# Kernel optimization log

Measured on AMD Instinct MI355X. Metric: run time of the kernel, lower is better.

Reference implementation:

```python
import jax, jax.numpy as jnp
import numpy as np

N_NODES = 50000
N_EDGES = 800000
NODE_F = 128
EDGE_F = 64
OUT_F = 128


def setup_inputs() -> dict:
    key = jax.random.key(0)
    k1, k2, k3, k4, k5 = jax.random.split(key, 5)
    x = jax.random.normal(k1, (N_NODES, NODE_F), dtype=jnp.float32)
    edge_index = jax.random.randint(k2, (2, N_EDGES), 0, N_NODES, dtype=jnp.int64)
    edge_attr = jax.random.normal(k3, (N_EDGES, EDGE_F), dtype=jnp.float32)
    # Linear(node_features + edge_features, out_features) params (torch default init scale)
    fan_in = NODE_F + EDGE_F
    bound = 1.0 / np.sqrt(fan_in)
    W = jax.random.uniform(k4, (fan_in, OUT_F), minval=-bound, maxval=bound, dtype=jnp.float32)
    b = jax.random.uniform(k5, (OUT_F,), minval=-bound, maxval=bound, dtype=jnp.float32)
    return {"x": x, "edge_index": edge_index, "edge_attr": edge_attr, "W": W, "b": b}


def reference(x, edge_index, edge_attr, W, b):
    # PyG source_to_target flow: x_j = x[src], aggregate at dst
    src = edge_index[0]
    dst = edge_index[1]
    x_j = x[src]                                   # [E, node_f] gather
    feats = jnp.concatenate([edge_attr, x_j], axis=1)  # [E, edge_f + node_f]
    msg = jax.nn.relu(feats @ W + b)               # [E, out_f] Linear + ReLU
    out = jax.ops.segment_sum(msg, dst, num_segments=x.shape[0])  # scatter-add
    return out
```

## Files before the change

### kernel.cpp

```cpp
#include <hip/hip_runtime.h>
#include <hip/hip_bf16.h>

#define N_NODES 50000
#define N_EDGES 800000
#define NODE_F  128
#define EDGE_F  64
#define OUT_F   128

#define NCH ((N_NODES + 255) / 256)
#define EPW 128
#define NRANGES (N_EDGES / EPW)

typedef __attribute__((ext_vector_type(8))) short short8;
typedef __attribute__((ext_vector_type(4))) short short4v;
typedef __attribute__((ext_vector_type(4))) float floatx4;

__device__ __forceinline__ unsigned short f2bf(float f) {
    unsigned int u = __float_as_uint(f);
    u += 0x7fffu + ((u >> 16) & 1u);
    return (unsigned short)(u >> 16);
}

__device__ __forceinline__ void load_bfrags(const float* __restrict__ W, int col, int quad,
                                            short8 bfr[2][8]) {
    #pragma unroll
    for (int kc = 0; kc < 2; ++kc) {
        #pragma unroll
        for (int ns = 0; ns < 8; ++ns) {
            const int n = ns * 16 + col;
            const int krow = kc * 32 + quad * 8;
            short8 v;
            #pragma unroll
            for (int j = 0; j < 8; ++j)
                v[j] = (short)f2bf(W[(krow + j) * OUT_F + n]);
            bfr[kc][ns] = v;
        }
    }
}

#define TILE_N1 32
#define N_NTILES ((N_NODES + TILE_N1 - 1) / TILE_N1)
#define LDS_STRIDE1 136

__global__ __launch_bounds__(256, 4) void node_kernel(
    const float* __restrict__ x,
    const float* __restrict__ W,
    const float* __restrict__ bias,
    float*       __restrict__ Y)
{
    __shared__ __align__(16) unsigned short xs[TILE_N1][LDS_STRIDE1];

    const int tid  = threadIdx.x;
    const int wave = tid >> 6;
    const int lane = tid & 63;
    const int col  = lane & 15;
    const int quad = lane >> 4;
    const int wbase = wave * 32;

    const float* __restrict__ Wx = W + EDGE_F * OUT_F;

    short8 bfr[4][2];
    #pragma unroll
    for (int kc = 0; kc < 4; ++kc) {
        #pragma unroll
        for (int ns = 0; ns < 2; ++ns) {
            const int n = wbase + ns * 16 + col;
            const int krow = kc * 32 + quad * 8;
            short8 v;
            #pragma unroll
            for (int j = 0; j < 8; ++j)
                v[j] = (short)f2bf(Wx[(krow + j) * OUT_F + n]);
            bfr[kc][ns] = v;
        }
    }
    const float b0 = bias[wbase + col];
    const float b1 = bias[wbase + 16 + col];

    for (int tile = blockIdx.x; tile < N_NTILES; tile += gridDim.x) {
        const int n0 = tile * TILE_N1;
        {
            const int e   = tid >> 3;
            const int sub = tid & 7;
            const int node = n0 + e;
            const float* __restrict__ xr = x + (size_t)node * NODE_F;
            #pragma unroll
            for (int i = 0; i < 4; ++i) {
                const int fi = sub + 8 * i;
                floatx4 v = {0.f, 0.f, 0.f, 0.f};
                if (node < N_NODES) v = *(const floatx4*)(xr + fi * 4);
                short4v sv;
                sv[0] = (short)f2bf(v[0]);
                sv[1] = (short)f2bf(v[1]);
                sv[2] = (short)f2bf(v[2]);
                sv[3] = (short)f2bf(v[3]);
                *(short4v*)&xs[e][fi * 4] = sv;
            }
        }
        __syncthreads();

        floatx4 acc[2][2] = {};
        #pragma unroll
        for (int kc = 0; kc < 4; ++kc) {
            short8 a0 = *(const short8*)&xs[col     ][kc * 32 + quad * 8];
            short8 a1 = *(const short8*)&xs[16 + col][kc * 32 + quad * 8];
            acc[0][0] = __builtin_amdgcn_mfma_f32_16x16x32_bf16(a0, bfr[kc][0], acc[0][0], 0, 0, 0);
            acc[0][1] = __builtin_amdgcn_mfma_f32_16x16x32_bf16(a0, bfr[kc][1], acc[0][1], 0, 0, 0);
            acc[1][0] = __builtin_amdgcn_mfma_f32_16x16x32_bf16(a1, bfr[kc][0], acc[1][0], 0, 0, 0);
            acc[1][1] = __builtin_amdgcn_mfma_f32_16x16x32_bf16(a1, bfr[kc][1], acc[1][1], 0, 0, 0);
        }

        #pragma unroll
        for (int ms = 0; ms < 2; ++ms) {
            #pragma unroll
            for (int r = 0; r < 4; ++r) {
                const int m = ms * 16 + quad * 4 + r;
                const int node = n0 + m;
                if (node < N_NODES) {
                    float* yrow = Y + (size_t)node * OUT_F + wbase;
                    yrow[col]      = acc[ms][0][r] + b0;
                    yrow[16 + col] = acc[ms][1][r] + b1;
                }
            }
        }
        __syncthreads();
    }
}

__global__ void hist_kernel(const int* __restrict__ edge_index, int* __restrict__ hist) {
    const int* dstp = edge_index + N_EDGES;
    for (int i = blockIdx.x * blockDim.x + threadIdx.x; i < N_EDGES;
         i += gridDim.x * blockDim.x)
        atomicAdd(&hist[dstp[i]], 1);
}

__global__ void scan1_kernel(const int* __restrict__ hist, int* __restrict__ chunkSum) {
    __shared__ int s[256];
    const int c = blockIdx.x, t = threadIdx.x, idx = c * 256 + t;
    s[t] = (idx < N_NODES) ? hist[idx] : 0;
    __syncthreads();
    for (int off = 128; off > 0; off >>= 1) {
        if (t < off) s[t] += s[t + off];
        __syncthreads();
    }
    if (t == 0) chunkSum[c] = s[0];
}

__global__ void scan2_kernel(const int* __restrict__ chunkSum, int* __restrict__ chunkBase) {
    __shared__ int s[256];
    const int t = threadIdx.x;
    s[t] = (t < NCH) ? chunkSum[t] : 0;
    __syncthreads();
    for (int off = 1; off < 256; off <<= 1) {
        int u = (t >= off) ? s[t - off] : 0;
        __syncthreads();
        s[t] += u;
        __syncthreads();
    }
    if (t < NCH) chunkBase[t] = (t == 0) ? 0 : s[t - 1];
}

__global__ void scan3_kernel(const int* __restrict__ hist, const int* __restrict__ chunkBase,
                             int* __restrict__ row_off, int* __restrict__ cursor) {
    __shared__ int s[256];
    const int c = blockIdx.x, t = threadIdx.x, idx = c * 256 + t;
    const int v = (idx < N_NODES) ? hist[idx] : 0;
    s[t] = v;
    __syncthreads();
    for (int off = 1; off < 256; off <<= 1) {
        int u = (t >= off) ? s[t - off] : 0;
        __syncthreads();
        s[t] += u;
        __syncthreads();
    }
    const int excl = s[t] - v + chunkBase[c];
    if (idx < N_NODES) { row_off[idx] = excl; cursor[idx] = excl; }
    if (c == 0 && t == 0) row_off[N_NODES] = N_EDGES;
}

__global__ void scatter_kernel(const int* __restrict__ edge_index,
                               int* __restrict__ cursor, int4* __restrict__ sorted) {
    const int* srcp = edge_index;
    const int* dstp = edge_index + N_EDGES;
    for (int i = blockIdx.x * blockDim.x + threadIdx.x; i < N_EDGES;
         i += gridDim.x * blockDim.x) {
        const int d = dstp[i];
        const int p = atomicAdd(&cursor[d], 1);
        sorted[p] = make_int4(i, srcp[i], d, 0);
    }
}

__device__ __forceinline__ int lbound(const int* __restrict__ ro, int target) {
    int lo = 0, hi = N_NODES;
    while (lo < hi) {
        const int mid = (lo + hi) >> 1;
        if (ro[mid] < target) lo = mid + 1; else hi = mid;
    }
    return lo;
}

__global__ __launch_bounds__(256, 3) void edge_gemm(
    const float* __restrict__ edge_attr,
    const float* __restrict__ W,
    const float* __restrict__ Y,
    const int*   __restrict__ row_off,
    const int4*  __restrict__ sorted,
    float*       __restrict__ out)
{
    __shared__ float CT[4][16][132];
    __shared__ int   drow[4][16];

    const int tid  = threadIdx.x;
    const int wave = tid >> 6;
    const int lane = tid & 63;
    const int col  = lane & 15;
    const int quad = lane >> 4;

    short8 bfr[2][8];
    load_bfrags(W, col, quad, bfr);

    const int gwave = blockIdx.x * 4 + wave;
    const int nw    = gridDim.x * 4;

    for (int rg = gwave; rg < NRANGES; rg += nw) {
        const int lo = lbound(row_off, rg * EPW);
        const int hi = lbound(row_off, (rg + 1) * EPW);
        const int eb = row_off[lo];
        const int ee = row_off[hi];
        if (eb >= ee) continue;

        int   cur = -1;
        float s0 = 0.f, s1 = 0.f;

        for (int t0 = eb; t0 < ee; t0 += 16) {
            const int cnt = min(16, ee - t0);

            int pa = t0 + col;
            if (pa >= ee) pa = ee - 1;
            const int4 me = sorted[pa];
            const float* __restrict__ ar = edge_attr + (size_t)me.x * EDGE_F;
            short8 a[2];
            #pragma unroll
            for (int kc = 0; kc < 2; ++kc) {
                floatx4 v0 = *(const floatx4*)(ar + kc * 32 + quad * 8);
                floatx4 v1 = *(const floatx4*)(ar + kc * 32 + quad * 8 + 4);
                short8 av;
                av[0] = (short)f2bf(v0[0]); av[1] = (short)f2bf(v0[1]);
                av[2] = (short)f2bf(v0[2]); av[3] = (short)f2bf(v0[3]);
                av[4] = (short)f2bf(v1[0]); av[5] = (short)f2bf(v1[1]);
                av[6] = (short)f2bf(v1[2]); av[7] = (short)f2bf(v1[3]);
                a[kc] = av;
            }

            if (lane < 16) drow[wave][lane] = (t0 + lane < ee) ? me.z : -1;

            const float* yrow[4];
            #pragma unroll
            for (int r = 0; r < 4; ++r) {
                int p = t0 + quad * 4 + r;
                if (p >= ee) p = ee - 1;
                yrow[r] = Y + (size_t)sorted[p].y * OUT_F;
            }

            floatx4 acc[8];
            #pragma unroll
            for (int ns = 0; ns < 8; ++ns) {
                #pragma unroll
                for (int r = 0; r < 4; ++r)
                    acc[ns][r] = yrow[r][ns * 16 + col];
            }

            #pragma unroll
            for (int kc = 0; kc < 2; ++kc) {
                #pragma unroll
                for (int ns = 0; ns < 8; ++ns)
                    acc[ns] = __builtin_amdgcn_mfma_f32_16x16x32_bf16(a[kc], bfr[kc][ns], acc[ns], 0, 0, 0);
            }

            #pragma unroll
            for (int ns = 0; ns < 8; ++ns) {
                #pragma unroll
                for (int r = 0; r < 4; ++r)
                    CT[wave][quad * 4 + r][ns * 16 + col] = fmaxf(acc[ns][r], 0.f);
            }
            __builtin_amdgcn_wave_barrier();

            for (int m = 0; m < cnt; ++m) {
                const int d = drow[wave][m];
                if (d != cur) {
                    if (cur >= 0) {
                        out[(size_t)cur * OUT_F + lane]      = s0;
                        out[(size_t)cur * OUT_F + 64 + lane] = s1;
                    }
                    cur = d; s0 = 0.f; s1 = 0.f;
                }
                s0 += CT[wave][m][lane];
                s1 += CT[wave][m][64 + lane];
            }
            __builtin_amdgcn_wave_barrier();
        }
        if (cur >= 0) {
            out[(size_t)cur * OUT_F + lane]      = s0;
            out[(size_t)cur * OUT_F + 64 + lane] = s1;
        }
    }
}

__global__ __launch_bounds__(256, 3) void edge_kernel_atomic(
    const float* __restrict__ edge_attr,
    const int*   __restrict__ edge_index,
    const float* __restrict__ W,
    const float* __restrict__ Y,
    float*       __restrict__ out)
{
    const int lane = threadIdx.x & 63;
    const int col  = lane & 15;
    const int quad = lane >> 4;

    short8 bfr[2][8];
    load_bfrags(W, col, quad, bfr);

    const int* __restrict__ srcp = edge_index;
    const int* __restrict__ dstp = edge_index + N_EDGES;

    const int gwave  = blockIdx.x * 4 + (threadIdx.x >> 6);
    const int nwaves = gridDim.x * 4;

    for (int t = gwave; t < N_EDGES / 16; t += nwaves) {
        const int e0 = t * 16;
        const float* __restrict__ ar = edge_attr + (size_t)(e0 + col) * EDGE_F;
        short8 a[2];
        #pragma unroll
        for (int kc = 0; kc < 2; ++kc) {
            floatx4 v0 = *(const floatx4*)(ar + kc * 32 + quad * 8);
            floatx4 v1 = *(const floatx4*)(ar + kc * 32 + quad * 8 + 4);
            short8 av;
            av[0] = (short)f2bf(v0[0]); av[1] = (short)f2bf(v0[1]);
            av[2] = (short)f2bf(v0[2]); av[3] = (short)f2bf(v0[3]);
            av[4] = (short)f2bf(v1[0]); av[5] = (short)f2bf(v1[1]);
            av[6] = (short)f2bf(v1[2]); av[7] = (short)f2bf(v1[3]);
            a[kc] = av;
        }
        int sr[4], dr[4];
        #pragma unroll
        for (int r = 0; r < 4; ++r) {
            sr[r] = srcp[e0 + quad * 4 + r];
            dr[r] = dstp[e0 + quad * 4 + r];
        }
        floatx4 acc[8];
        #pragma unroll
        for (int ns = 0; ns < 8; ++ns)
            #pragma unroll
            for (int r = 0; r < 4; ++r)
                acc[ns][r] = Y[(size_t)sr[r] * OUT_F + ns * 16 + col];
        #pragma unroll
        for (int kc = 0; kc < 2; ++kc)
            #pragma unroll
            for (int ns = 0; ns < 8; ++ns)
                acc[ns] = __builtin_amdgcn_mfma_f32_16x16x32_bf16(a[kc], bfr[kc][ns], acc[ns], 0, 0, 0);
        #pragma unroll
        for (int ns = 0; ns < 8; ++ns)
            #pragma unroll
            for (int r = 0; r < 4; ++r) {
                const float v = acc[ns][r];
                if (v > 0.0f)
                    atomicAdd(out + (size_t)dr[r] * OUT_F + ns * 16 + col, v);
            }
    }
}

extern "C" void kernel_launch(void* const* d_in, const int* in_sizes, int n_in,
                              void* d_out, int out_size, void* d_ws, size_t ws_size,
                              hipStream_t stream) {
    const float* x          = (const float*)d_in[0];
    const int*   edge_index = (const int*)  d_in[1];
    const float* edge_attr  = (const float*)d_in[2];
    const float* W          = (const float*)d_in[3];
    const float* bias       = (const float*)d_in[4];
    float*       out        = (float*)d_out;

    float* Y        = (float*)d_ws;
    int4*  sorted   = (int4*)(Y + (size_t)N_NODES * OUT_F);
    int*   hist     = (int*)(sorted + N_EDGES);
    int*   chunkSum = hist + N_NODES;
    int*   chunkBase= chunkSum + 256;
    int*   row_off  = chunkBase + 256;
    int*   cursor   = row_off + N_NODES + 1;
    const size_t needed = (size_t)((char*)(cursor + N_NODES) - (char*)d_ws);

    hipMemsetAsync(out, 0, (size_t)out_size * sizeof(float), stream);
    node_kernel<<<dim3(512), dim3(256), 0, stream>>>(x, W, bias, Y);

    if (ws_size < needed) {
        edge_kernel_atomic<<<dim3(1024), dim3(256), 0, stream>>>(edge_attr, edge_index, W, Y, out);
        return;
    }

    hipMemsetAsync(hist, 0, (size_t)N_NODES * sizeof(int), stream);
    hist_kernel   <<<dim3(2048), dim3(256), 0, stream>>>(edge_index, hist);
    scan1_kernel  <<<dim3(NCH),  dim3(256), 0, stream>>>(hist, chunkSum);
    scan2_kernel  <<<dim3(1),    dim3(256), 0, stream>>>(chunkSum, chunkBase);
    scan3_kernel  <<<dim3(NCH),  dim3(256), 0, stream>>>(hist, chunkBase, row_off, cursor);
    scatter_kernel<<<dim3(2048), dim3(256), 0, stream>>>(edge_index, cursor, sorted);
    edge_gemm     <<<dim3(1563), dim3(256), 0, stream>>>(edge_attr, W, Y, row_off, sorted, out);
}
```

Measured before the change: 516.2 us.

## Split edge GEMM columns across wave pairs, precompute range bounds, prefetch next tile

Each destination-sorted edge range is now handled by two waves, each computing 64 of the 128 output columns. This halves per-wave B fragments, accumulators and LDS, which allows a higher occupancy bound. The per-wave binary searches for range bounds move into a separate range_kernel. Inside the loop, dst ids are read via readlane instead of LDS, src indices are shuffled from the already loaded sorted entry, and the next tile's sorted entry and edge_attr are loaded early. The cost is duplicated edge_attr/sorted loads across the two waves and one extra small kernel launch.

```diff
diff --git a/kernel.cpp b/kernel.cpp
--- a/kernel.cpp
+++ b/kernel.cpp
@@ -19,23 +19,6 @@
     unsigned int u = __float_as_uint(f);
     u += 0x7fffu + ((u >> 16) & 1u);
     return (unsigned short)(u >> 16);
-}
-
-__device__ __forceinline__ void load_bfrags(const float* __restrict__ W, int col, int quad,
-                                            short8 bfr[2][8]) {
-    #pragma unroll
-    for (int kc = 0; kc < 2; ++kc) {
-        #pragma unroll
-        for (int ns = 0; ns < 8; ++ns) {
-            const int n = ns * 16 + col;
-            const int krow = kc * 32 + quad * 8;
-            short8 v;
-            #pragma unroll
-            for (int j = 0; j < 8; ++j)
-                v[j] = (short)f2bf(W[(krow + j) * OUT_F + n]);
-            bfr[kc][ns] = v;
-        }
-    }
 }
 
 #define TILE_N1 32
@@ -177,6 +160,20 @@
     if (c == 0 && t == 0) row_off[N_NODES] = N_EDGES;
 }
 
+__device__ __forceinline__ int lbound(const int* __restrict__ ro, int target) {
+    int lo = 0, hi = N_NODES;
+    while (lo < hi) {
+        const int mid = (lo + hi) >> 1;
+        if (ro[mid] < target) lo = mid + 1; else hi = mid;
+    }
+    return lo;
+}
+
+__global__ void range_kernel(const int* __restrict__ row_off, int* __restrict__ range_lo) {
+    const int rg = blockIdx.x * blockDim.x + threadIdx.x;
+    if (rg <= NRANGES) range_lo[rg] = lbound(row_off, rg * EPW);
+}
+
 __global__ void scatter_kernel(const int* __restrict__ edge_index,
                                int* __restrict__ cursor, int4* __restrict__ sorted) {
     const int* srcp = edge_index;
@@ -189,56 +186,54 @@
     }
 }
 
-__device__ __forceinline__ int lbound(const int* __restrict__ ro, int target) {
-    int lo = 0, hi = N_NODES;
-    while (lo < hi) {
-        const int mid = (lo + hi) >> 1;
-        if (ro[mid] < target) lo = mid + 1; else hi = mid;
-    }
-    return lo;
-}
-
-__global__ __launch_bounds__(256, 3) void edge_gemm(
+__global__ __launch_bounds__(256, 4) void edge_gemm(
     const float* __restrict__ edge_attr,
     const float* __restrict__ W,
     const float* __restrict__ Y,
     const int*   __restrict__ row_off,
+    const int*   __restrict__ range_lo,
     const int4*  __restrict__ sorted,
     float*       __restrict__ out)
 {
-    __shared__ float CT[4][16][132];
-    __shared__ int   drow[4][16];
+    __shared__ float CT[4][16][68];
 
     const int tid  = threadIdx.x;
     const int wave = tid >> 6;
     const int lane = tid & 63;
     const int col  = lane & 15;
     const int quad = lane >> 4;
-
-    short8 bfr[2][8];
-    load_bfrags(W, col, quad, bfr);
-
-    const int gwave = blockIdx.x * 4 + wave;
-    const int nw    = gridDim.x * 4;
-
-    for (int rg = gwave; rg < NRANGES; rg += nw) {
-        const int lo = lbound(row_off, rg * EPW);
-        const int hi = lbound(row_off, (rg + 1) * EPW);
-        const int eb = row_off[lo];
-        const int ee = row_off[hi];
+    const int p    = wave & 1;
+
+    short8 bfr[2][4];
+    #pragma unroll
+    for (int kc = 0; kc < 2; ++kc) {
+        #pragma unroll
+        for (int ns = 0; ns < 4; ++ns) {
+            const int n = p * 64 + ns * 16 + col;
+            const int krow = kc * 32 + quad * 8;
+            short8 v;
+            #pragma unroll
+            for (int j = 0; j < 8; ++j)
+                v[j] = (short)f2bf(W[(krow + j) * OUT_F + n]);
+            bfr[kc][ns] = v;
+        }
+    }
+
+    const int grange = blockIdx.x * 2 + (wave >> 1);
+    const int stride = gridDim.x * 2;
+
+    for (int rg = grange; rg < NRANGES; rg += stride) {
+        const int eb = row_off[range_lo[rg]];
+        const int ee = row_off[range_lo[rg + 1]];
         if (eb >= ee) continue;
 
         int   cur = -1;
-        float s0 = 0.f, s1 = 0.f;
-
-        for (int t0 = eb; t0 < ee; t0 += 16) {
-            const int cnt = min(16, ee - t0);
-
-            int pa = t0 + col;
-            if (pa >= ee) pa = ee - 1;
-            const int4 me = sorted[pa];
+        float s   = 0.f;
+
+        int4 me = sorted[min(eb + col, ee - 1)];
+        short8 a[2];
+        {
             const float* __restrict__ ar = edge_attr + (size_t)me.x * EDGE_F;
-            short8 a[2];
             #pragma unroll
             for (int kc = 0; kc < 2; ++kc) {
                 floatx4 v0 = *(const floatx4*)(ar + kc * 32 + quad * 8);
@@ -250,58 +245,73 @@
                 av[6] = (short)f2bf(v1[2]); av[7] = (short)f2bf(v1[3]);
                 a[kc] = av;
             }
-
-            if (lane < 16) drow[wave][lane] = (t0 + lane < ee) ? me.z : -1;
-
-            const float* yrow[4];
+        }
+
+        for (int t0 = eb; t0 < ee; t0 += 16) {
+            floatx4 acc[4];
             #pragma unroll
             for (int r = 0; r < 4; ++r) {
-                int p = t0 + quad * 4 + r;
-                if (p >= ee) p = ee - 1;
-                yrow[r] = Y + (size_t)sorted[p].y * OUT_F;
-            }
-
-            floatx4 acc[8];
-            #pragma unroll
-            for (int ns = 0; ns < 8; ++ns) {
+                const int src = __shfl(me.y, quad * 4 + r);
+                const float* __restrict__ yr = Y + (size_t)src * OUT_F + p * 64;
                 #pragma unroll
-                for (int r = 0; r < 4; ++r)
-                    acc[ns][r] = yrow[r][ns * 16 + col];
+                for (int ns = 0; ns < 4; ++ns)
+                    acc[ns][r] = yr[ns * 16 + col];
             }
 
             #pragma unroll
             for (int kc = 0; kc < 2; ++kc) {
                 #pragma unroll
-                for (int ns = 0; ns < 8; ++ns)
+                for (int ns = 0; ns < 4; ++ns)
                     acc[ns] = __builtin_amdgcn_mfma_f32_16x16x32_bf16(a[kc], bfr[kc][ns], acc[ns], 0, 0, 0);
             }
 
             #pragma unroll
-            for (int ns = 0; ns < 8; ++ns) {
+            for (int r = 0; r < 4; ++r) {
+                const bool rvalid = (t0 + quad * 4 + r) < ee;
                 #pragma unroll
-                for (int r = 0; r < 4; ++r)
-                    CT[wave][quad * 4 + r][ns * 16 + col] = fmaxf(acc[ns][r], 0.f);
+                for (int ns = 0; ns < 4; ++ns)
+                    CT[wave][quad * 4 + r][ns * 16 + col] =
+                        rvalid ? fmaxf(acc[ns][r], 0.f) : 0.f;
             }
             __builtin_amdgcn_wave_barrier();
 
-            for (int m = 0; m < cnt; ++m) {
-                const int d = drow[wave][m];
+            const int t1 = t0 + 16;
+            int4 me2;
+            if (t1 < ee) me2 = sorted[min(t1 + col, ee - 1)];
+
+            float cv[16];
+            #pragma unroll
+            for (int m = 0; m < 16; ++m) cv[m] = CT[wave][m][lane];
+
+            #pragma unroll
+            for (int m = 0; m < 16; ++m) {
+                const int d = __builtin_amdgcn_readlane(me.z, m);
                 if (d != cur) {
-                    if (cur >= 0) {
-                        out[(size_t)cur * OUT_F + lane]      = s0;
-                        out[(size_t)cur * OUT_F + 64 + lane] = s1;
-                    }
-                    cur = d; s0 = 0.f; s1 = 0.f;
+                    if (cur >= 0) out[(size_t)cur * OUT_F + p * 64 + lane] = s;
+                    cur = d; s = 0.f;
                 }
-                s0 += CT[wave][m][lane];
-                s1 += CT[wave][m][64 + lane];
-            }
+                s += cv[m];
+            }
+            cur = __builtin_amdgcn_readfirstlane(cur);
             __builtin_amdgcn_wave_barrier();
-        }
-        if (cur >= 0) {
-            out[(size_t)cur * OUT_F + lane]      = s0;
-            out[(size_t)cur * OUT_F + 64 + lane] = s1;
-        }
+
+            if (t1 < ee) {
+                me = me2;
+                const float* __restrict__ ar = edge_attr + (size_t)me.x * EDGE_F;
+                #pragma unroll
+                for (int kc = 0; kc < 2; ++kc) {
+                    floatx4 v0 = *(const floatx4*)(ar + kc * 32 + quad * 8);
+                    floatx4 v1 = *(const floatx4*)(ar + kc * 32 + quad * 8 + 4);
+                    short8 av;
+                    av[0] = (short)f2bf(v0[0]); av[1] = (short)f2bf(v0[1]);
+                    av[2] = (short)f2bf(v0[2]); av[3] = (short)f2bf(v0[3]);
+                    av[4] = (short)f2bf(v1[0]); av[5] = (short)f2bf(v1[1]);
+                    av[6] = (short)f2bf(v1[2]); av[7] = (short)f2bf(v1[3]);
+                    a[kc] = av;
+                }
+            }
+        }
+        if (cur >= 0) out[(size_t)cur * OUT_F + p * 64 + lane] = s;
     }
 }
 
@@ -317,7 +327,18 @@
     const int quad = lane >> 4;
 
     short8 bfr[2][8];
-    load_bfrags(W, col, quad, bfr);
+    #pragma unroll
+    for (int kc = 0; kc < 2; ++kc)
+        #pragma unroll
+        for (int ns = 0; ns < 8; ++ns) {
+            const int n = ns * 16 + col;
+            const int krow = kc * 32 + quad * 8;
+            short8 v;
+            #pragma unroll
+            for (int j = 0; j < 8; ++j)
+                v[j] = (short)f2bf(W[(krow + j) * OUT_F + n]);
+            bfr[kc][ns] = v;
+        }
 
     const int* __restrict__ srcp = edge_index;
     const int* __restrict__ dstp = edge_index + N_EDGES;
@@ -385,7 +406,8 @@
     int*   chunkBase= chunkSum + 256;
     int*   row_off  = chunkBase + 256;
     int*   cursor   = row_off + N_NODES + 1;
-    const size_t needed = (size_t)((char*)(cursor + N_NODES) - (char*)d_ws);
+    int*   range_lo = cursor + N_NODES;
+    const size_t needed = (size_t)((char*)(range_lo + NRANGES + 1) - (char*)d_ws);
 
     hipMemsetAsync(out, 0, (size_t)out_size * sizeof(float), stream);
     node_kernel<<<dim3(512), dim3(256), 0, stream>>>(x, W, bias, Y);
@@ -400,6 +422,8 @@
     scan1_kernel  <<<dim3(NCH),  dim3(256), 0, stream>>>(hist, chunkSum);
     scan2_kernel  <<<dim3(1),    dim3(256), 0, stream>>>(chunkSum, chunkBase);
     scan3_kernel  <<<dim3(NCH),  dim3(256), 0, stream>>>(hist, chunkBase, row_off, cursor);
+    range_kernel  <<<dim3((NRANGES + 256) / 256), dim3(256), 0, stream>>>(row_off, range_lo);
     scatter_kernel<<<dim3(2048), dim3(256), 0, stream>>>(edge_index, cursor, sorted);
-    edge_gemm     <<<dim3(1563), dim3(256), 0, stream>>>(edge_attr, W, Y, row_off, sorted, out);
-}
+    edge_gemm     <<<dim3((NRANGES + 1) / 2), dim3(256), 0, stream>>>(
+        edge_attr, W, Y, row_off, range_lo, sorted, out);
+}
```

After: 488.0 us. 5.4% less time.
